# Optimization experiments

Hardware: AMD Instinct MI355X
Metric: run time of the kernel (lower is better)

Reference implementation:

```python
import jax, jax.numpy as jnp
import numpy as np

B, T, E, H = 256, 256, 384, 64

def setup_inputs() -> dict:
    key = jax.random.key(0)
    ks = jax.random.split(key, 4)
    s = 1.0 / np.sqrt(E)
    return {
        "x":  jax.random.normal(ks[0], (B, T, E), dtype=jnp.float32),
        "Wq": jax.random.normal(ks[1], (E, H), dtype=jnp.float32) * s,
        "bq": jnp.zeros((H,), dtype=jnp.float32),
        "Wk": jax.random.normal(ks[2], (E, H), dtype=jnp.float32) * s,
        "bk": jnp.zeros((H,), dtype=jnp.float32),
        "Wv": jax.random.normal(ks[3], (E, H), dtype=jnp.float32) * s,
        "bv": jnp.zeros((H,), dtype=jnp.float32),
    }

def reference(x, Wq, bq, Wk, bk, Wv, bv):
    # QKV projections: [B,T,E] @ [E,H] -> [B,T,H]
    q = x @ Wq + bq
    k = x @ Wk + bk
    v = x @ Wv + bv
    # attention scores (NOTE: original has no 1/sqrt(d) scaling)
    wei = jnp.einsum('bth,bsh->bts', q, k)  # [B,T,T]
    causal = jnp.tril(jnp.ones((T, T), dtype=bool))
    wei = jnp.where(causal, wei, -jnp.inf)
    wei = jax.nn.softmax(wei, axis=-1)
    # dropout is identity in eval mode
    out = jnp.einsum('bts,bsh->bth', wei, v)  # [B,T,H]
    return out
```

## Files before the change

### kernel.cpp

```cpp
#include <hip/hip_runtime.h>
#include <math.h>

#define Bb 256
#define Tt 256
#define Ee 384
#define Hh 64

typedef __attribute__((ext_vector_type(8))) short bf16x8;
typedef __attribute__((ext_vector_type(4))) float f32x4;

__device__ inline short f2bf(float f) {
    unsigned u = __float_as_uint(f);
    u += 0x7FFFu + ((u >> 16) & 1);
    return (short)(u >> 16);
}
__device__ inline float bf2f(short s) {
    return __uint_as_float(((unsigned)(unsigned short)s) << 16);
}

#define MFMA16(a, b, c) __builtin_amdgcn_mfma_f32_16x16x32_bf16((a), (b), (c), 0, 0, 0)

#define A_HI 0
#define A_LO 16384
#define B_HI 32768
#define B_LO 45056
#define K_HI 0
#define K_LO 32768
#define VF   65536
#define QH   98304
#define QL   116736
#define PBASE 98304
#define SMEM_BYTES 135168

__global__ __launch_bounds__(1024) void head_fused(
    const float* __restrict__ x,
    const float* __restrict__ Wq, const float* __restrict__ bq,
    const float* __restrict__ Wk, const float* __restrict__ bk,
    const float* __restrict__ Wv, const float* __restrict__ bv,
    float* __restrict__ out)
{
    __shared__ __align__(16) unsigned char smem[SMEM_BYTES];

    const int b    = blockIdx.x;
    const int tid  = threadIdx.x;
    const int w    = tid >> 6;
    const int lane = tid & 63;
    const int quad = lane >> 4;
    const int nl   = lane & 15;
    const int wi   = w >> 1;
    const int wj   = w & 1;

    f32x4 acc0[6], acc1[6];
    #pragma unroll
    for (int i = 0; i < 6; ++i) { acc0[i] = (f32x4){0,0,0,0}; acc1[i] = (f32x4){0,0,0,0}; }

    const float4* x4 = reinterpret_cast<const float4*>(x + (size_t)b * Tt * Ee);

    const int At  = ((tid >> 6) << 4) + (tid & 15);
    const int Ako = (tid >> 4) & 3;
    const float4* xsrc = x4 + At * 96 + Ako * 2;
    const int wtile = tid >> 6, weo = (tid >> 4) & 3, wn0 = tid & 15;
    const int wcol  = wtile * 16 + wn0;
    const float* Wsel = (wcol < 64) ? Wq : ((wcol < 128) ? Wk : Wv);
    const float* wsrc = Wsel + (wcol & 63) + weo * 8 * 64;

    float4 pa0 = xsrc[0], pa1 = xsrc[1];
    float pw[8];
    if (tid < 768) {
        #pragma unroll
        for (int j = 0; j < 8; ++j) pw[j] = wsrc[j * 64];
    }

    for (int ec = 0; ec < 12; ++ec) {
        __syncthreads();

        {
            float v[8] = {pa0.x, pa0.y, pa0.z, pa0.w, pa1.x, pa1.y, pa1.z, pa1.w};
            bf16x8 hi8, lo8;
            #pragma unroll
            for (int j = 0; j < 8; ++j) {
                short h = f2bf(v[j]);
                hi8[j] = h;
                lo8[j] = f2bf(v[j] - bf2f(h));
            }
            *reinterpret_cast<bf16x8*>(smem + A_HI + tid * 16) = hi8;
            *reinterpret_cast<bf16x8*>(smem + A_LO + tid * 16) = lo8;
        }
        if (tid < 768) {
            bf16x8 hi8, lo8;
            #pragma unroll
            for (int j = 0; j < 8; ++j) {
                short h = f2bf(pw[j]);
                hi8[j] = h;
                lo8[j] = f2bf(pw[j] - bf2f(h));
            }
            *reinterpret_cast<bf16x8*>(smem + B_HI + tid * 16) = hi8;
            *reinterpret_cast<bf16x8*>(smem + B_LO + tid * 16) = lo8;
        }
        __syncthreads();

        if (ec < 11) {
            pa0 = xsrc[(ec + 1) * 8];
            pa1 = xsrc[(ec + 1) * 8 + 1];
            if (tid < 768) {
                #pragma unroll
                for (int j = 0; j < 8; ++j) pw[j] = wsrc[(ec + 1) * 2048 + j * 64];
            }
        }

        int ao = (2 * wi) * 1024 + lane * 16;
        bf16x8 a0h = *reinterpret_cast<bf16x8*>(smem + A_HI + ao);
        bf16x8 a0l = *reinterpret_cast<bf16x8*>(smem + A_LO + ao);
        bf16x8 a1h = *reinterpret_cast<bf16x8*>(smem + A_HI + ao + 1024);
        bf16x8 a1l = *reinterpret_cast<bf16x8*>(smem + A_LO + ao + 1024);
        #pragma unroll
        for (int ct = 0; ct < 6; ++ct) {
            int tb = (wj * 6 + ct) * 1024 + lane * 16;
            bf16x8 bh = *reinterpret_cast<bf16x8*>(smem + B_HI + tb);
            bf16x8 bl = *reinterpret_cast<bf16x8*>(smem + B_LO + tb);
            acc0[ct] = MFMA16(a0h, bh, acc0[ct]);
            acc0[ct] = MFMA16(a0l, bh, acc0[ct]);
            acc0[ct] = MFMA16(a0h, bl, acc0[ct]);
            acc1[ct] = MFMA16(a1h, bh, acc1[ct]);
            acc1[ct] = MFMA16(a1l, bh, acc1[ct]);
            acc1[ct] = MFMA16(a1h, bl, acc1[ct]);
        }
    }
    __syncthreads();

    #pragma unroll
    for (int ct = 0; ct < 6; ++ct) {
        int col = (wj * 6 + ct) * 16 + nl;
        float bias = (col < 64) ? bq[col] : (col < 128 ? bk[col - 64] : bv[col - 128]);
        #pragma unroll
        for (int r = 0; r < 4; ++r) { acc0[ct][r] += bias; acc1[ct][r] += bias; }
    }

    #pragma unroll
    for (int ct = 0; ct < 6; ++ct) {
        int col = (wj * 6 + ct) * 16 + nl;
        #pragma unroll
        for (int rt = 0; rt < 2; ++rt) {
            #pragma unroll
            for (int r = 0; r < 4; ++r) {
                float val = (rt ? acc1[ct] : acc0[ct])[r];
                int s = wi * 32 + rt * 16 + quad * 4 + r;
                if (col >= 64 && col < 128) {
                    int h = col - 64;
                    int addr = ((s >> 4) * 2 + (h >> 5)) * 1024
                             + ((((h & 31) >> 3) * 16 + (s & 15)) * 8 + (h & 7)) * 2;
                    short hi = f2bf(val);
                    short lo = f2bf(val - bf2f(hi));
                    *reinterpret_cast<short*>(smem + K_HI + addr) = hi;
                    *reinterpret_cast<short*>(smem + K_LO + addr) = lo;
                } else if (col >= 128) {
                    int h = col - 128, sl = s & 31;
                    int addr = ((s >> 5) * 4 + (h >> 4)) * 1024
                             + (((sl >> 3) * 16 + (h & 15)) * 8 + (sl & 7)) * 2;
                    *reinterpret_cast<short*>(smem + VF + addr) = f2bf(val);
                }
            }
        }
    }

    auto writeQ = [&]() {
        #pragma unroll
        for (int ct = 0; ct < 4; ++ct) {
            #pragma unroll
            for (int rt = 0; rt < 2; ++rt) {
                #pragma unroll
                for (int r = 0; r < 4; ++r) {
                    float val = (rt ? acc1[ct] : acc0[ct])[r];
                    int s = wi * 32 + rt * 16 + quad * 4 + r;
                    int rloc = s & 127;
                    int h = ct * 16 + nl;
                    short hi = f2bf(val);
                    short lo = f2bf(val - bf2f(hi));
                    *reinterpret_cast<short*>(smem + QH + (rloc * 72 + h) * 2) = hi;
                    *reinterpret_cast<short*>(smem + QL + (rloc * 72 + h) * 2) = lo;
                }
            }
        }
    };
    bf16x8 qh0, qh1, ql0, ql1;
    auto readQ = [&]() {
        int rloc = (16 * w + nl) & 127;
        int base = rloc * 144;
        qh0 = *reinterpret_cast<bf16x8*>(smem + QH + base + quad * 16);
        qh1 = *reinterpret_cast<bf16x8*>(smem + QH + base + 64 + quad * 16);
        ql0 = *reinterpret_cast<bf16x8*>(smem + QL + base + quad * 16);
        ql1 = *reinterpret_cast<bf16x8*>(smem + QL + base + 64 + quad * 16);
    };

    if (wj == 0 && wi < 4) writeQ();
    __syncthreads();
    if (w < 8) readQ();
    __syncthreads();
    if (wj == 0 && wi >= 4) writeQ();
    __syncthreads();
    if (w >= 8) readQ();
    __syncthreads();

    f32x4 oacc[4];
    #pragma unroll
    for (int i = 0; i < 4; ++i) oacc[i] = (f32x4){0,0,0,0};
    float lsum = 0.f;
    const int t0 = w * 16;
    unsigned char* pb = smem + PBASE + w * 1344;
    const int npairs = (w >> 1) + 1;

    for (int p = 0; p < npairs; ++p) {
        #pragma unroll
        for (int hf = 0; hf < 2; ++hf) {
            int st = 2 * p + hf;
            f32x4 s0 = (f32x4){0,0,0,0}, s1 = (f32x4){0,0,0,0};
            int kb = st * 2048 + lane * 16;
            bf16x8 kh0 = *reinterpret_cast<bf16x8*>(smem + K_HI + kb);
            bf16x8 kh1 = *reinterpret_cast<bf16x8*>(smem + K_HI + kb + 1024);
            bf16x8 kl0 = *reinterpret_cast<bf16x8*>(smem + K_LO + kb);
            bf16x8 kl1 = *reinterpret_cast<bf16x8*>(smem + K_LO + kb + 1024);
            s0 = MFMA16(qh0, kh0, s0);
            s1 = MFMA16(qh1, kh1, s1);
            s0 = MFMA16(ql0, kh0, s0);
            s1 = MFMA16(ql1, kh1, s1);
            s0 = MFMA16(qh0, kl0, s0);
            s1 = MFMA16(qh1, kl1, s1);
            int sg = st * 16 + nl;
            #pragma unroll
            for (int r = 0; r < 4; ++r) {
                int tg = t0 + quad * 4 + r;
                float sv = s0[r] + s1[r];
                float pv = (sg <= tg) ? __expf(sv) : 0.f;
                *reinterpret_cast<short*>(pb + ((quad * 4 + r) * 40 + hf * 16 + nl) * 2) = f2bf(pv);
            }
        }
        asm volatile("s_waitcnt lgkmcnt(0)" ::: "memory");
        bf16x8 pa = *reinterpret_cast<bf16x8*>(pb + (nl * 40 + quad * 8) * 2);
        float ls = 0.f;
        #pragma unroll
        for (int j = 0; j < 8; ++j) ls += bf2f(pa[j]);
        ls += __shfl_xor(ls, 16);
        ls += __shfl_xor(ls, 32);
        lsum += ls;
        int vb = p * 4096 + lane * 16;
        #pragma unroll
        for (int nt = 0; nt < 4; ++nt) {
            bf16x8 vf = *reinterpret_cast<bf16x8*>(smem + VF + vb + nt * 1024);
            oacc[nt] = MFMA16(pa, vf, oacc[nt]);
        }
    }

    float* lb_ = reinterpret_cast<float*>(pb + 1280);
    if (lane < 16) lb_[lane] = lsum;
    asm volatile("s_waitcnt lgkmcnt(0)" ::: "memory");
    float* ob = out + (size_t)b * Tt * Hh + (size_t)t0 * Hh;
    #pragma unroll
    for (int r = 0; r < 4; ++r) {
        float inv = 1.0f / lb_[quad * 4 + r];
        #pragma unroll
        for (int nt = 0; nt < 4; ++nt)
            ob[(quad * 4 + r) * 64 + nt * 16 + nl] = oacc[nt][r] * inv;
    }
}

extern "C" void kernel_launch(void* const* d_in, const int* in_sizes, int n_in,
                              void* d_out, int out_size, void* d_ws, size_t ws_size,
                              hipStream_t stream) {
    const float* x  = (const float*)d_in[0];
    const float* Wq = (const float*)d_in[1];
    const float* bq = (const float*)d_in[2];
    const float* Wk = (const float*)d_in[3];
    const float* bk = (const float*)d_in[4];
    const float* Wv = (const float*)d_in[5];
    const float* bv = (const float*)d_in[6];
    float* out = (float*)d_out;
    hipLaunchKernelGGL(head_fused, dim3(Bb), dim3(1024), 0, stream,
                       x, Wq, bq, Wk, bk, Wv, bv, out);
}
```

Baseline: 185.0 us.

## Pre-split weights into MFMA fragments and double-buffer x tiles in LDS

A small prep kernel converts Wq/Wk/Wv into hi/lo bf16 MFMA fragment layout in workspace once per call. The fused kernel then reads B fragments straight from global (L2-resident) into registers instead of converting and staging them through LDS in every block. The x A-tiles are double-buffered in LDS so each iteration needs one barrier instead of two. The warp tiling changes to 4 row tiles x 3 column tiles per wave, which raises A-fragment reuse. The cost is an extra kernel launch and global loads of the weights inside the loop.

After: 186.3 us. Within noise of the previous version (+0.7%).

```diff
diff --git a/kernel.cpp b/kernel.cpp
--- a/kernel.cpp
+++ b/kernel.cpp
@@ -20,10 +20,8 @@
 
 #define MFMA16(a, b, c) __builtin_amdgcn_mfma_f32_16x16x32_bf16((a), (b), (c), 0, 0, 0)
 
-#define A_HI 0
-#define A_LO 16384
-#define B_HI 32768
-#define B_LO 45056
+#define WLO_OFF 147456
+
 #define K_HI 0
 #define K_LO 32768
 #define VF   65536
@@ -32,11 +30,36 @@
 #define PBASE 98304
 #define SMEM_BYTES 135168
 
+__global__ __launch_bounds__(256) void prep_w(
+    const float* __restrict__ Wq, const float* __restrict__ Wk,
+    const float* __restrict__ Wv, unsigned char* __restrict__ wsp)
+{
+    int u = blockIdx.x * 256 + threadIdx.x;
+    if (u >= 9216) return;
+    int frag = u >> 6;
+    int lu   = u & 63;
+    int ec   = frag / 12, tct = frag - ec * 12;
+    int koct = lu >> 4, n = lu & 15;
+    int col  = tct * 16 + n;
+    const float* Wm = (col < 64) ? Wq : ((col < 128) ? Wk : Wv);
+    int c = col & 63;
+    bf16x8 hi8, lo8;
+    #pragma unroll
+    for (int j = 0; j < 8; ++j) {
+        float v = Wm[(ec * 32 + koct * 8 + j) * 64 + c];
+        short h = f2bf(v);
+        hi8[j] = h;
+        lo8[j] = f2bf(v - bf2f(h));
+    }
+    *reinterpret_cast<bf16x8*>(wsp + frag * 1024 + lu * 16) = hi8;
+    *reinterpret_cast<bf16x8*>(wsp + WLO_OFF + frag * 1024 + lu * 16) = lo8;
+}
+
 __global__ __launch_bounds__(1024) void head_fused(
     const float* __restrict__ x,
-    const float* __restrict__ Wq, const float* __restrict__ bq,
-    const float* __restrict__ Wk, const float* __restrict__ bk,
-    const float* __restrict__ Wv, const float* __restrict__ bv,
+    const float* __restrict__ bq, const float* __restrict__ bk,
+    const float* __restrict__ bv,
+    const unsigned char* __restrict__ wsp,
     float* __restrict__ out)
 {
     __shared__ __align__(16) unsigned char smem[SMEM_BYTES];
@@ -47,34 +70,47 @@
     const int lane = tid & 63;
     const int quad = lane >> 4;
     const int nl   = lane & 15;
-    const int wi   = w >> 1;
-    const int wj   = w & 1;
-
-    f32x4 acc0[6], acc1[6];
-    #pragma unroll
-    for (int i = 0; i < 6; ++i) { acc0[i] = (f32x4){0,0,0,0}; acc1[i] = (f32x4){0,0,0,0}; }
+    const int ri   = w >> 2;
+    const int cj   = w & 3;
+
+    f32x4 acc[4][3];
+    #pragma unroll
+    for (int i = 0; i < 4; ++i)
+        #pragma unroll
+        for (int j = 0; j < 3; ++j) acc[i][j] = (f32x4){0,0,0,0};
 
     const float4* x4 = reinterpret_cast<const float4*>(x + (size_t)b * Tt * Ee);
 
     const int At  = ((tid >> 6) << 4) + (tid & 15);
     const int Ako = (tid >> 4) & 3;
     const float4* xsrc = x4 + At * 96 + Ako * 2;
-    const int wtile = tid >> 6, weo = (tid >> 4) & 3, wn0 = tid & 15;
-    const int wcol  = wtile * 16 + wn0;
-    const float* Wsel = (wcol < 64) ? Wq : ((wcol < 128) ? Wk : Wv);
-    const float* wsrc = Wsel + (wcol & 63) + weo * 8 * 64;
 
     float4 pa0 = xsrc[0], pa1 = xsrc[1];
-    float pw[8];
-    if (tid < 768) {
-        #pragma unroll
-        for (int j = 0; j < 8; ++j) pw[j] = wsrc[j * 64];
-    }
+    {
+        float v[8] = {pa0.x, pa0.y, pa0.z, pa0.w, pa1.x, pa1.y, pa1.z, pa1.w};
+        bf16x8 hi8, lo8;
+        #pragma unroll
+        for (int j = 0; j < 8; ++j) {
+            short h = f2bf(v[j]);
+            hi8[j] = h;
+            lo8[j] = f2bf(v[j] - bf2f(h));
+        }
+        *reinterpret_cast<bf16x8*>(smem + tid * 16) = hi8;
+        *reinterpret_cast<bf16x8*>(smem + 16384 + tid * 16) = lo8;
+    }
+    pa0 = xsrc[8]; pa1 = xsrc[9];
 
     for (int ec = 0; ec < 12; ++ec) {
         __syncthreads();
-
-        {
+        const int bufr = (ec & 1) * 32768;
+        bf16x8 bh[3], bl[3];
+        #pragma unroll
+        for (int ct = 0; ct < 3; ++ct) {
+            size_t o = (size_t)(ec * 12 + cj * 3 + ct) * 1024 + lane * 16;
+            bh[ct] = *reinterpret_cast<const bf16x8*>(wsp + o);
+            bl[ct] = *reinterpret_cast<const bf16x8*>(wsp + WLO_OFF + o);
+        }
+        if (ec < 11) {
             float v[8] = {pa0.x, pa0.y, pa0.z, pa0.w, pa1.x, pa1.y, pa1.z, pa1.w};
             bf16x8 hi8, lo8;
             #pragma unroll
@@ -83,68 +119,46 @@
                 hi8[j] = h;
                 lo8[j] = f2bf(v[j] - bf2f(h));
             }
-            *reinterpret_cast<bf16x8*>(smem + A_HI + tid * 16) = hi8;
-            *reinterpret_cast<bf16x8*>(smem + A_LO + tid * 16) = lo8;
-        }
-        if (tid < 768) {
-            bf16x8 hi8, lo8;
-            #pragma unroll
-            for (int j = 0; j < 8; ++j) {
-                short h = f2bf(pw[j]);
-                hi8[j] = h;
-                lo8[j] = f2bf(pw[j] - bf2f(h));
-            }
-            *reinterpret_cast<bf16x8*>(smem + B_HI + tid * 16) = hi8;
-            *reinterpret_cast<bf16x8*>(smem + B_LO + tid * 16) = lo8;
-        }
-        __syncthreads();
-
-        if (ec < 11) {
-            pa0 = xsrc[(ec + 1) * 8];
-            pa1 = xsrc[(ec + 1) * 8 + 1];
-            if (tid < 768) {
-                #pragma unroll
-                for (int j = 0; j < 8; ++j) pw[j] = wsrc[(ec + 1) * 2048 + j * 64];
-            }
-        }
-
-        int ao = (2 * wi) * 1024 + lane * 16;
-        bf16x8 a0h = *reinterpret_cast<bf16x8*>(smem + A_HI + ao);
-        bf16x8 a0l = *reinterpret_cast<bf16x8*>(smem + A_LO + ao);
-        bf16x8 a1h = *reinterpret_cast<bf16x8*>(smem + A_HI + ao + 1024);
-        bf16x8 a1l = *reinterpret_cast<bf16x8*>(smem + A_LO + ao + 1024);
-        #pragma unroll
-        for (int ct = 0; ct < 6; ++ct) {
-            int tb = (wj * 6 + ct) * 1024 + lane * 16;
-            bf16x8 bh = *reinterpret_cast<bf16x8*>(smem + B_HI + tb);
-            bf16x8 bl = *reinterpret_cast<bf16x8*>(smem + B_LO + tb);
-            acc0[ct] = MFMA16(a0h, bh, acc0[ct]);
-            acc0[ct] = MFMA16(a0l, bh, acc0[ct]);
-            acc0[ct] = MFMA16(a0h, bl, acc0[ct]);
-            acc1[ct] = MFMA16(a1h, bh, acc1[ct]);
-            acc1[ct] = MFMA16(a1l, bh, acc1[ct]);
-            acc1[ct] = MFMA16(a1h, bl, acc1[ct]);
-        }
-    }
-    __syncthreads();
-
-    #pragma unroll
-    for (int ct = 0; ct < 6; ++ct) {
-        int col = (wj * 6 + ct) * 16 + nl;
+            int nb = (1 - (ec & 1)) * 32768;
+            *reinterpret_cast<bf16x8*>(smem + nb + tid * 16) = hi8;
+            *reinterpret_cast<bf16x8*>(smem + nb + 16384 + tid * 16) = lo8;
+        }
+        if (ec < 10) { pa0 = xsrc[(ec + 2) * 8]; pa1 = xsrc[(ec + 2) * 8 + 1]; }
+
+        #pragma unroll
+        for (int rt = 0; rt < 4; ++rt) {
+            int ao = bufr + (4 * ri + rt) * 1024 + lane * 16;
+            bf16x8 ah = *reinterpret_cast<bf16x8*>(smem + ao);
+            bf16x8 al = *reinterpret_cast<bf16x8*>(smem + ao + 16384);
+            #pragma unroll
+            for (int ct = 0; ct < 3; ++ct) {
+                acc[rt][ct] = MFMA16(ah, bh[ct], acc[rt][ct]);
+                acc[rt][ct] = MFMA16(al, bh[ct], acc[rt][ct]);
+                acc[rt][ct] = MFMA16(ah, bl[ct], acc[rt][ct]);
+            }
+        }
+    }
+    __syncthreads();
+
+    #pragma unroll
+    for (int ct = 0; ct < 3; ++ct) {
+        int col = (cj * 3 + ct) * 16 + nl;
         float bias = (col < 64) ? bq[col] : (col < 128 ? bk[col - 64] : bv[col - 128]);
         #pragma unroll
-        for (int r = 0; r < 4; ++r) { acc0[ct][r] += bias; acc1[ct][r] += bias; }
-    }
-
-    #pragma unroll
-    for (int ct = 0; ct < 6; ++ct) {
-        int col = (wj * 6 + ct) * 16 + nl;
-        #pragma unroll
-        for (int rt = 0; rt < 2; ++rt) {
+        for (int rt = 0; rt < 4; ++rt)
+            #pragma unroll
+            for (int r = 0; r < 4; ++r) acc[rt][ct][r] += bias;
+    }
+
+    #pragma unroll
+    for (int ct = 0; ct < 3; ++ct) {
+        int col = (cj * 3 + ct) * 16 + nl;
+        #pragma unroll
+        for (int rt = 0; rt < 4; ++rt) {
             #pragma unroll
             for (int r = 0; r < 4; ++r) {
-                float val = (rt ? acc1[ct] : acc0[ct])[r];
-                int s = wi * 32 + rt * 16 + quad * 4 + r;
+                float val = acc[rt][ct][r];
+                int s = ri * 64 + rt * 16 + quad * 4 + r;
                 if (col >= 64 && col < 128) {
                     int h = col - 64;
                     int addr = ((s >> 4) * 2 + (h >> 5)) * 1024
@@ -163,21 +177,23 @@
         }
     }
 
-    auto writeQ = [&]() {
-        #pragma unroll
-        for (int ct = 0; ct < 4; ++ct) {
-            #pragma unroll
-            for (int rt = 0; rt < 2; ++rt) {
+    auto writeQhalf = [&](int half) {
+        #pragma unroll
+        for (int ct = 0; ct < 3; ++ct) {
+            int col = (cj * 3 + ct) * 16 + nl;
+            if (col < 64) {
                 #pragma unroll
-                for (int r = 0; r < 4; ++r) {
-                    float val = (rt ? acc1[ct] : acc0[ct])[r];
-                    int s = wi * 32 + rt * 16 + quad * 4 + r;
-                    int rloc = s & 127;
-                    int h = ct * 16 + nl;
-                    short hi = f2bf(val);
-                    short lo = f2bf(val - bf2f(hi));
-                    *reinterpret_cast<short*>(smem + QH + (rloc * 72 + h) * 2) = hi;
-                    *reinterpret_cast<short*>(smem + QL + (rloc * 72 + h) * 2) = lo;
+                for (int rt = 0; rt < 4; ++rt) {
+                    #pragma unroll
+                    for (int r = 0; r < 4; ++r) {
+                        float val = acc[rt][ct][r];
+                        int s = ri * 64 + rt * 16 + quad * 4 + r;
+                        int rloc = s & 127;
+                        short hi = f2bf(val);
+                        short lo = f2bf(val - bf2f(hi));
+                        *reinterpret_cast<short*>(smem + QH + (rloc * 72 + col) * 2) = hi;
+                        *reinterpret_cast<short*>(smem + QL + (rloc * 72 + col) * 2) = lo;
+                    }
                 }
             }
         }
@@ -192,11 +208,11 @@
         ql1 = *reinterpret_cast<bf16x8*>(smem + QL + base + 64 + quad * 16);
     };
 
-    if (wj == 0 && wi < 4) writeQ();
+    if (ri < 2) writeQhalf(0);
     __syncthreads();
     if (w < 8) readQ();
     __syncthreads();
-    if (wj == 0 && wi >= 4) writeQ();
+    if (ri >= 2) writeQhalf(1);
     __syncthreads();
     if (w >= 8) readQ();
     __syncthreads();
@@ -274,6 +290,8 @@
     const float* Wv = (const float*)d_in[5];
     const float* bv = (const float*)d_in[6];
     float* out = (float*)d_out;
+    unsigned char* wsp = (unsigned char*)d_ws;
+    hipLaunchKernelGGL(prep_w, dim3(36), dim3(256), 0, stream, Wq, Wk, Wv, wsp);
     hipLaunchKernelGGL(head_fused, dim3(Bb), dim3(1024), 0, stream,
-                       x, Wq, bq, Wk, bk, Wv, bv, out);
-}
+                       x, bq, bk, bv, wsp, out);
+}
```
